# Kernel optimization log

Measured on AMD Instinct MI355X. Metric: run time of the kernel, lower is better.

## Reference

```python
import jax, jax.numpy as jnp
import numpy as np

N_NODES = 10000
N_GRAPHS = 64
NEG_SLOPE = 0.2
EPS = 1e-16


def gat_conv(x, src, dst, W, a_src, a_dst, bias, heads, out_ch, num_nodes):
    """PyG GATConv (shared lin, add_self_loops already applied to src/dst)."""
    xl = (x @ W).reshape(num_nodes, heads, out_ch)          # [N,H,C]
    alpha_s = jnp.einsum('nhc,hc->nh', xl, a_src)           # [N,H]
    alpha_d = jnp.einsum('nhc,hc->nh', xl, a_dst)           # [N,H]
    e = jax.nn.leaky_relu(alpha_s[src] + alpha_d[dst], NEG_SLOPE)  # [E,H]
    # segment softmax over incoming edges of each destination node
    emax = jax.ops.segment_max(e, dst, num_segments=num_nodes)
    emax = jnp.where(jnp.isfinite(emax), emax, 0.0)
    ee = jnp.exp(e - emax[dst])
    denom = jax.ops.segment_sum(ee, dst, num_segments=num_nodes)
    alpha = ee / (denom[dst] + EPS)                         # [E,H]
    msg = xl[src] * alpha[:, :, None]                       # [E,H,C]
    out = jax.ops.segment_sum(msg, dst, num_segments=num_nodes)  # [N,H,C]
    return out.reshape(num_nodes, heads * out_ch) + bias


def setup_inputs() -> dict:
    key = jax.random.key(0)
    ks = jax.random.split(key, 16)
    H, C, IN = 8, 128, 128
    x = jax.random.normal(ks[0], (N_NODES, IN), jnp.float32)
    edge_index = jax.random.randint(ks[1], (2, 320000), 0, N_NODES, jnp.int64)
    batch = jnp.sort(jax.random.randint(ks[2], (N_NODES,), 0, N_GRAPHS, jnp.int64))
    g = lambda k, shp, fan: jax.random.normal(k, shp, jnp.float32) * (1.0 / np.sqrt(fan))
    return {
        'x': x, 'edge_index': edge_index, 'batch': batch,
        'W1': g(ks[3], (IN, H * C), IN),
        'a_src1': g(ks[4], (H, C), C), 'a_dst1': g(ks[5], (H, C), C),
        'b1': jnp.zeros((H * C,), jnp.float32),
        'W2': g(ks[6], (H * C, C), H * C),
        'a_src2': g(ks[7], (1, C), C), 'a_dst2': g(ks[8], (1, C), C),
        'b2': jnp.zeros((C,), jnp.float32),
        'lin1_w': g(ks[9], (C, 128), C), 'lin1_b': jnp.zeros((128,), jnp.float32),
        'lin2_w': g(ks[10], (128, 1), 128), 'lin2_b': jnp.zeros((1,), jnp.float32),
    }


def reference(x, edge_index, batch, W1, a_src1, a_dst1, b1, W2, a_src2, a_dst2, b2,
              lin1_w, lin1_b, lin2_w, lin2_b):
    loops = jnp.arange(N_NODES, dtype=edge_index.dtype)
    src = jnp.concatenate([edge_index[0], loops])
    dst = jnp.concatenate([edge_index[1], loops])
    h = jax.nn.elu(gat_conv(x, src, dst, W1, a_src1, a_dst1, b1, 8, 128, N_NODES))
    h = jax.nn.elu(gat_conv(h, src, dst, W2, a_src2, a_dst2, b2, 1, 128, N_NODES))
    # global mean pool over graphs
    sums = jax.ops.segment_sum(h, batch, num_segments=N_GRAPHS)
    cnts = jax.ops.segment_sum(jnp.ones((N_NODES,), h.dtype), batch, num_segments=N_GRAPHS)
    pooled = sums / jnp.maximum(cnts, 1.0)[:, None]         # [G,128]
    z = jax.nn.relu(pooled @ lin1_w + lin1_b)
    return (z @ lin2_w + lin2_b).squeeze(1)                 # [G]
```

## Files before the change

### kernel.cpp

```cpp
#include <hip/hip_runtime.h>
#include <math.h>

#define N_NODES 10000
#define N_GRAPHS 64
#define E_RAW 320000
#define E_ALL (E_RAW + N_NODES)
#define NEG_SLOPE 0.2f
#define EPS 1e-16f
#define CAP 192

typedef unsigned short ushort_t;
typedef short short8 __attribute__((ext_vector_type(8)));
typedef float floatx4 __attribute__((ext_vector_type(4)));

static __device__ __forceinline__ float bfl(unsigned u) {
  union { unsigned u; float f; } v; v.u = u << 16; return v.f;
}
static __device__ __forceinline__ float bfh(unsigned u) {
  union { unsigned u; float f; } v; v.u = u & 0xFFFF0000u; return v.f;
}
static __device__ __forceinline__ ushort_t f2bf(float f) {
  union { float f; unsigned u; } v; v.f = f;
  unsigned r = v.u + 0x7FFFu + ((v.u >> 16) & 1u);
  return (ushort_t)(r >> 16);
}

static __device__ __forceinline__ void load16_lds(const ushort_t* gp, ushort_t* ldsbase, int lane) {
#if __has_builtin(__builtin_amdgcn_global_load_lds)
  __builtin_amdgcn_global_load_lds((const __attribute__((address_space(1))) void*)gp,
                                   (__attribute__((address_space(3))) void*)ldsbase, 16, 0, 0);
#else
  *(uint4*)(ldsbase + lane * 8) = *(const uint4*)gp;
#endif
}

static __device__ __forceinline__ void swz_one(const float* __restrict__ W,
                                               ushort_t* __restrict__ Wsw,
                                               int idx, int K, int N) {
  int NT = N >> 4;
  int lane = idx & 63, tile = idx >> 6;
  int nt = tile % NT, kt = tile / NT;
  int n = nt * 16 + (lane & 15);
  int kb = kt * 32 + (lane >> 4) * 8;
  ushort4 lo, hi;
  lo.x = f2bf(W[(size_t)(kb + 0) * N + n]); lo.y = f2bf(W[(size_t)(kb + 1) * N + n]);
  lo.z = f2bf(W[(size_t)(kb + 2) * N + n]); lo.w = f2bf(W[(size_t)(kb + 3) * N + n]);
  hi.x = f2bf(W[(size_t)(kb + 4) * N + n]); hi.y = f2bf(W[(size_t)(kb + 5) * N + n]);
  hi.z = f2bf(W[(size_t)(kb + 6) * N + n]); hi.w = f2bf(W[(size_t)(kb + 7) * N + n]);
  *(ushort4*)(Wsw + (size_t)idx * 8) = lo;
  *(ushort4*)(Wsw + (size_t)idx * 8 + 4) = hi;
}

__global__ __launch_bounds__(1024) void prep_k(const float* __restrict__ x,
                                               const int* __restrict__ batch,
                                               const float* __restrict__ W1,
                                               const float* __restrict__ W2,
                                               ushort_t* __restrict__ xb,
                                               ushort_t* __restrict__ W1sw,
                                               ushort_t* __restrict__ W2sw,
                                               float* __restrict__ zero0,
                                               int* __restrict__ poolcnt) {
  __shared__ int shm[N_GRAPHS];
  const int b = blockIdx.x, t = threadIdx.x;
  if (b < 49) {
    int i4 = b * 1024 + t;
    if (i4 < 49548) *(float4*)(zero0 + i4 * 4) = make_float4(0.f, 0.f, 0.f, 0.f);
  } else if (b == 49) {
    if (t < N_GRAPHS) shm[t] = 0;
    __syncthreads();
    for (int n = t; n < N_NODES; n += 1024) atomicAdd(&shm[batch[n]], 1);
    __syncthreads();
    if (t < N_GRAPHS) poolcnt[t] = shm[t];
  } else if (b < 363) {
    int i4 = (b - 50) * 1024 + t;
    if (i4 < 320000) {
      float4 v = *(const float4*)(x + (size_t)i4 * 4);
      ushort4 o;
      o.x = f2bf(v.x); o.y = f2bf(v.y); o.z = f2bf(v.z); o.w = f2bf(v.w);
      *(ushort4*)(xb + (size_t)i4 * 4) = o;
    }
  } else if (b < 379) {
    int idx = (b - 363) * 1024 + t;
    if (idx < 16384) swz_one(W1, W1sw, idx, 128, 1024);
  } else {
    int idx = (b - 379) * 1024 + t;
    if (idx < 16384) swz_one(W2, W2sw, idx, 1024, 128);
  }
}

__global__ __launch_bounds__(256) void g1f_k(const ushort_t* __restrict__ A,
                                             const ushort_t* __restrict__ Bsw,
                                             ushort_t* __restrict__ Cb,
                                             const float* __restrict__ aS,
                                             const float* __restrict__ aD,
                                             float* __restrict__ asO,
                                             float* __restrict__ adO,
                                             const int* __restrict__ ei,
                                             int* __restrict__ degc,
                                             int* __restrict__ csr) {
  __shared__ ushort_t Albuf[32 * 512];
  __shared__ float epi[4][16][68];
  const int bid = blockIdx.x, t = threadIdx.x;
  if (bid >= 632) {
    int e = (bid - 632) * 256 + t;
    if (e < E_ALL) {
      int s, d;
      if (e < E_RAW) { s = ei[e]; d = ei[E_RAW + e]; }
      else           { s = d = e - E_RAW; }
      int pos = atomicAdd(&degc[d], 1);
      if (pos < CAP) csr[d * CAP + pos] = s;
    }
    return;
  }
  const int M = N_NODES, K = 128, NT = 64;
  const int lane = t & 63, w = t >> 6;
  const int wm = w >> 1, wn = w & 1;
  const int m0 = (bid >> 3) * 128;
  const int n0 = (bid & 7) * 128;
  const int g = lane >> 4, l16 = lane & 15;

  #pragma unroll
  for (int i = 0; i < 8; i++) {
    int tile = w * 8 + i;
    int mtl = tile >> 2, kt = tile & 3;
    int r = m0 + mtl * 16 + l16; r = r < M ? r : M - 1;
    load16_lds(A + (size_t)r * K + kt * 32 + g * 8, &Albuf[tile * 512], lane);
  }
  __syncthreads();

  floatx4 acc[4][4] = {};
  #pragma unroll
  for (int kt = 0; kt < 4; kt++) {
    short8 a[4], b[4];
    #pragma unroll
    for (int mi = 0; mi < 4; mi++)
      a[mi] = *(const short8*)&Albuf[(((wm * 4 + mi) * 4 + kt) * 64 + lane) * 8];
    #pragma unroll
    for (int ni = 0; ni < 4; ni++) {
      int nt = (n0 >> 4) + wn * 4 + ni;
      b[ni] = *(const short8*)(Bsw + ((size_t)(kt * NT + nt) * 64 + lane) * 8);
    }
    #pragma unroll
    for (int mi = 0; mi < 4; mi++)
      #pragma unroll
      for (int ni = 0; ni < 4; ni++)
        acc[mi][ni] = __builtin_amdgcn_mfma_f32_16x16x32_bf16(a[mi], b[ni], acc[mi][ni], 0, 0, 0);
  }

  const int h = bid & 7;
  const int r = lane >> 2, c0 = (lane & 3) * 16;
  const int colh = wn * 64 + c0;
  float asc[16], adc[16];
  #pragma unroll
  for (int c = 0; c < 16; c++) { asc[c] = aS[h * 128 + colh + c]; adc[c] = aD[h * 128 + colh + c]; }
  #pragma unroll
  for (int mi = 0; mi < 4; mi++) {
    #pragma unroll
    for (int ni = 0; ni < 4; ni++)
      #pragma unroll
      for (int reg = 0; reg < 4; reg++)
        epi[w][g * 4 + reg][ni * 16 + l16] = acc[mi][ni][reg];
    float4 v0 = *(float4*)&epi[w][r][c0];
    float4 v1 = *(float4*)&epi[w][r][c0 + 4];
    float4 v2 = *(float4*)&epi[w][r][c0 + 8];
    float4 v3 = *(float4*)&epi[w][r][c0 + 12];
    float vr[16] = {v0.x,v0.y,v0.z,v0.w, v1.x,v1.y,v1.z,v1.w,
                    v2.x,v2.y,v2.z,v2.w, v3.x,v3.y,v3.z,v3.w};
    int grow = m0 + wm * 64 + mi * 16 + r;
    float sp = 0.f, dp = 0.f;
    ushort_t hv[16];
    #pragma unroll
    for (int c = 0; c < 16; c++) {
      sp = fmaf(vr[c], asc[c], sp);
      dp = fmaf(vr[c], adc[c], dp);
      hv[c] = f2bf(vr[c]);
    }
    sp += __shfl_xor(sp, 1); sp += __shfl_xor(sp, 2);
    dp += __shfl_xor(dp, 1); dp += __shfl_xor(dp, 2);
    if (grow < M) {
      uint4 u0, u1;
      u0.x = (unsigned)hv[0] | ((unsigned)hv[1] << 16);
      u0.y = (unsigned)hv[2] | ((unsigned)hv[3] << 16);
      u0.z = (unsigned)hv[4] | ((unsigned)hv[5] << 16);
      u0.w = (unsigned)hv[6] | ((unsigned)hv[7] << 16);
      u1.x = (unsigned)hv[8] | ((unsigned)hv[9] << 16);
      u1.y = (unsigned)hv[10] | ((unsigned)hv[11] << 16);
      u1.z = (unsigned)hv[12] | ((unsigned)hv[13] << 16);
      u1.w = (unsigned)hv[14] | ((unsigned)hv[15] << 16);
      ushort_t* cp = Cb + (size_t)grow * 1024 + (bid & 7) * 128 + wn * 64 + c0;
      *(uint4*)cp = u0;
      *(uint4*)(cp + 8) = u1;
      if ((lane & 3) == 0) {
        atomicAdd(&asO[grow * 8 + h], sp);
        atomicAdd(&adO[grow * 8 + h], dp);
      }
    }
  }
}

__global__ __launch_bounds__(256) void gemm2_k(const ushort_t* __restrict__ A,
                                               const ushort_t* __restrict__ Bsw,
                                               ushort_t* __restrict__ Cb,
                                               const float* __restrict__ aS,
                                               const float* __restrict__ aD,
                                               float* __restrict__ asO,
                                               float* __restrict__ adO) {
  const int M = N_NODES, K = 1024, NT = 8;
  __shared__ ushort_t Albuf[8 * 512];
  __shared__ float epi[4][16][68];
  const int t = threadIdx.x, lane = t & 63, w = t >> 6;
  const int wm = w >> 1, wn = w & 1;
  const int mb0 = blockIdx.x * 32;
  const int g = lane >> 4, l16 = lane & 15;

  floatx4 acc[4] = {};
  for (int ch = 0; ch < 8; ch++) {
    #pragma unroll
    for (int i = 0; i < 2; i++) {
      int tile = w * 2 + i;
      int mtl = tile >> 2, kt = tile & 3;
      int r = mb0 + mtl * 16 + l16; r = r < M ? r : M - 1;
      load16_lds(A + (size_t)r * K + (ch * 4 + kt) * 32 + g * 8, &Albuf[tile * 512], lane);
    }
    __syncthreads();
    #pragma unroll
    for (int ks = 0; ks < 4; ks++) {
      short8 a = *(const short8*)&Albuf[(((wm * 4 + ks)) * 64 + lane) * 8];
      #pragma unroll
      for (int ni = 0; ni < 4; ni++) {
        int nt = wn * 4 + ni, ktg = ch * 4 + ks;
        short8 b = *(const short8*)(Bsw + ((size_t)(ktg * NT + nt) * 64 + lane) * 8);
        acc[ni] = __builtin_amdgcn_mfma_f32_16x16x32_bf16(a, b, acc[ni], 0, 0, 0);
      }
    }
    __syncthreads();
  }

  const int r = lane >> 2, c0 = (lane & 3) * 16;
  const int colh = wn * 64 + c0;
  float asc[16], adc[16];
  #pragma unroll
  for (int c = 0; c < 16; c++) { asc[c] = aS[colh + c]; adc[c] = aD[colh + c]; }
  #pragma unroll
  for (int ni = 0; ni < 4; ni++)
    #pragma unroll
    for (int reg = 0; reg < 4; reg++)
      epi[w][g * 4 + reg][ni * 16 + l16] = acc[ni][reg];
  float4 v0 = *(float4*)&epi[w][r][c0];
  float4 v1 = *(float4*)&epi[w][r][c0 + 4];
  float4 v2 = *(float4*)&epi[w][r][c0 + 8];
  float4 v3 = *(float4*)&epi[w][r][c0 + 12];
  float vr[16] = {v0.x,v0.y,v0.z,v0.w, v1.x,v1.y,v1.z,v1.w,
                  v2.x,v2.y,v2.z,v2.w, v3.x,v3.y,v3.z,v3.w};
  int grow = mb0 + wm * 16 + r;
  float sp = 0.f, dp = 0.f;
  ushort_t hv[16];
  #pragma unroll
  for (int c = 0; c < 16; c++) {
    sp = fmaf(vr[c], asc[c], sp);
    dp = fmaf(vr[c], adc[c], dp);
    hv[c] = f2bf(vr[c]);
  }
  sp += __shfl_xor(sp, 1); sp += __shfl_xor(sp, 2);
  dp += __shfl_xor(dp, 1); dp += __shfl_xor(dp, 2);
  if (grow < M) {
    uint4 u0, u1;
    u0.x = (unsigned)hv[0] | ((unsigned)hv[1] << 16);
    u0.y = (unsigned)hv[2] | ((unsigned)hv[3] << 16);
    u0.z = (unsigned)hv[4] | ((unsigned)hv[5] << 16);
    u0.w = (unsigned)hv[6] | ((unsigned)hv[7] << 16);
    u1.x = (unsigned)hv[8] | ((unsigned)hv[9] << 16);
    u1.y = (unsigned)hv[10] | ((unsigned)hv[11] << 16);
    u1.z = (unsigned)hv[12] | ((unsigned)hv[13] << 16);
    u1.w = (unsigned)hv[14] | ((unsigned)hv[15] << 16);
    ushort_t* cp = Cb + (size_t)grow * 128 + colh;
    *(uint4*)cp = u0;
    *(uint4*)(cp + 8) = u1;
    if ((lane & 3) == 0) {
      atomicAdd(&asO[grow], sp);
      atomicAdd(&adO[grow], dp);
    }
  }
}

__global__ __launch_bounds__(64) void agg1_k(const ushort_t* __restrict__ xlb,
                                             const float* __restrict__ as1,
                                             const float* __restrict__ ad1,
                                             const float* __restrict__ b1,
                                             const int* __restrict__ degc,
                                             const int* __restrict__ csr,
                                             ushort_t* __restrict__ out) {
  const int bid = blockIdx.x, t = threadIdx.x;
  const int h = bid & 7, dst = bid >> 3;
  int deg = degc[dst]; deg = deg < CAP ? deg : CAP;
  const int beg = dst * CAP;
  const int degp = (deg + 7) & ~7;
  __shared__ uint2 pr[CAP];
  float adh = ad1[dst * 8 + h];
  if (deg <= 64) {
    bool act = t < deg;
    int s = act ? csr[beg + t] : 0;
    float lg = -1e30f;
    if (act) {
      float v = as1[s * 8 + h] + adh;
      lg = v > 0.f ? v : NEG_SLOPE * v;
    }
    float pm = lg;
    #pragma unroll
    for (int off = 32; off; off >>= 1) pm = fmaxf(pm, __shfl_xor(pm, off));
    float ex = act ? __expf(lg - pm) : 0.f;
    float ps = ex;
    #pragma unroll
    for (int off = 32; off; off >>= 1) ps += __shfl_xor(ps, off);
    float inv = 1.0f / (ps + EPS);
    if (t < degp) pr[t] = act ? make_uint2((unsigned)(s * 2048), __float_as_uint(ex * inv))
                              : make_uint2(0u, 0u);
    __syncthreads();
  } else {
    __shared__ int ssg[CAP];
    __shared__ float alg[CAP];
    for (int e = t; e < deg; e += 64) ssg[e] = csr[beg + e];
    __syncthreads();
    float pm = -1e30f;
    for (int e = t; e < deg; e += 64) {
      float v = as1[ssg[e] * 8 + h] + adh;
      v = v > 0.f ? v : NEG_SLOPE * v;
      alg[e] = v;
      pm = fmaxf(pm, v);
    }
    #pragma unroll
    for (int off = 32; off; off >>= 1) pm = fmaxf(pm, __shfl_xor(pm, off));
    __syncthreads();
    float ps = 0.f;
    for (int e = t; e < deg; e += 64) ps += __expf(alg[e] - pm);
    #pragma unroll
    for (int off = 32; off; off >>= 1) ps += __shfl_xor(ps, off);
    float inv = 1.0f / (ps + EPS);
    for (int e = t; e < deg; e += 64)
      pr[e] = make_uint2((unsigned)(ssg[e] * 2048), __float_as_uint(__expf(alg[e] - pm) * inv));
    for (int e = deg + t; e < degp; e += 64) pr[e] = make_uint2(0u, 0u);
    __syncthreads();
  }
  const int g = t >> 4, sub = t & 15;
  const char* xbase = (const char*)xlb + (h * 256 + 16 * sub);
  float acc[8] = {};
  for (int e0 = 0; e0 < degp; e0 += 8) {
    uint2 pA = pr[e0 + g];
    uint2 pB = pr[e0 + 4 + g];
    uint4 qA = *(const uint4*)(xbase + pA.x);
    uint4 qB = *(const uint4*)(xbase + pB.x);
    float aA = __uint_as_float(pA.y), aB = __uint_as_float(pB.y);
    acc[0] = fmaf(aA, bfl(qA.x), acc[0]); acc[1] = fmaf(aA, bfh(qA.x), acc[1]);
    acc[2] = fmaf(aA, bfl(qA.y), acc[2]); acc[3] = fmaf(aA, bfh(qA.y), acc[3]);
    acc[4] = fmaf(aA, bfl(qA.z), acc[4]); acc[5] = fmaf(aA, bfh(qA.z), acc[5]);
    acc[6] = fmaf(aA, bfl(qA.w), acc[6]); acc[7] = fmaf(aA, bfh(qA.w), acc[7]);
    acc[0] = fmaf(aB, bfl(qB.x), acc[0]); acc[1] = fmaf(aB, bfh(qB.x), acc[1]);
    acc[2] = fmaf(aB, bfl(qB.y), acc[2]); acc[3] = fmaf(aB, bfh(qB.y), acc[3]);
    acc[4] = fmaf(aB, bfl(qB.z), acc[4]); acc[5] = fmaf(aB, bfh(qB.z), acc[5]);
    acc[6] = fmaf(aB, bfl(qB.w), acc[6]); acc[7] = fmaf(aB, bfh(qB.w), acc[7]);
  }
  const bool hi32 = (t & 32) != 0;
  float s0, s1, s2, s3;
  {
    float m0 = hi32 ? acc[4] : acc[0], o0 = hi32 ? acc[0] : acc[4];
    float m1 = hi32 ? acc[5] : acc[1], o1 = hi32 ? acc[1] : acc[5];
    float m2 = hi32 ? acc[6] : acc[2], o2 = hi32 ? acc[2] : acc[6];
    float m3 = hi32 ? acc[7] : acc[3], o3 = hi32 ? acc[3] : acc[7];
    s0 = m0 + __shfl_xor(o0, 32);
    s1 = m1 + __shfl_xor(o1, 32);
    s2 = m2 + __shfl_xor(o2, 32);
    s3 = m3 + __shfl_xor(o3, 32);
  }
  const bool hi16 = (t & 16) != 0;
  float r0, r1;
  {
    float m0 = hi16 ? s2 : s0, o0 = hi16 ? s0 : s2;
    float m1 = hi16 ? s3 : s1, o1 = hi16 ? s1 : s3;
    r0 = m0 + __shfl_xor(o0, 16);
    r1 = m1 + __shfl_xor(o1, 16);
  }
  const int c = 8 * sub + 2 * g;
  const int o = h * 128 + c;
  float2 bb = *(const float2*)(b1 + o);
  float v0 = r0 + bb.x;
  float v1 = r1 + bb.y;
  v0 = v0 > 0.f ? v0 : (__expf(v0) - 1.0f);
  v1 = v1 > 0.f ? v1 : (__expf(v1) - 1.0f);
  unsigned up = (unsigned)f2bf(v0) | ((unsigned)f2bf(v1) << 16);
  *(unsigned*)(out + (size_t)dst * 1024 + o) = up;
}

__global__ __launch_bounds__(64) void agg2_k(const ushort_t* __restrict__ xlb2,
                                             const float* __restrict__ as2,
                                             const float* __restrict__ ad2,
                                             const float* __restrict__ b2,
                                             const int* __restrict__ degc,
                                             const int* __restrict__ csr,
                                             const int* __restrict__ batch,
                                             float* __restrict__ poolsum) {
  int dst = blockIdx.x, t = threadIdx.x;
  int deg = degc[dst]; deg = deg < CAP ? deg : CAP;
  int beg = dst * CAP;
  const int degp = (deg + 7) & ~7;
  float adv = ad2[dst];
  __shared__ uint2 pr[CAP];
  if (deg <= 64) {
    bool act = t < deg;
    int s = act ? csr[beg + t] : 0;
    float lg = -1e30f;
    if (act) {
      float v = as2[s] + adv;
      lg = v > 0.f ? v : NEG_SLOPE * v;
    }
    float pm = lg;
    #pragma unroll
    for (int off = 32; off; off >>= 1) pm = fmaxf(pm, __shfl_xor(pm, off));
    float ex = act ? __expf(lg - pm) : 0.f;
    float ps = ex;
    #pragma unroll
    for (int off = 32; off; off >>= 1) ps += __shfl_xor(ps, off);
    float inv = 1.0f / (ps + EPS);
    if (t < degp) pr[t] = act ? make_uint2((unsigned)(s * 256), __float_as_uint(ex * inv))
                              : make_uint2(0u, 0u);
    __syncthreads();
  } else {
    __shared__ int ssg[CAP];
    __shared__ float alg[CAP];
    for (int e = t; e < deg; e += 64) ssg[e] = csr[beg + e];
    __syncthreads();
    float pm = -1e30f;
    for (int e = t; e < deg; e += 64) {
      float v = as2[ssg[e]] + adv;
      v = v > 0.f ? v : NEG_SLOPE * v;
      alg[e] = v;
      pm = fmaxf(pm, v);
    }
    #pragma unroll
    for (int off = 32; off; off >>= 1) pm = fmaxf(pm, __shfl_xor(pm, off));
    __syncthreads();
    float ps = 0.f;
    for (int e = t; e < deg; e += 64) ps += __expf(alg[e] - pm);
    #pragma unroll
    for (int off = 32; off; off >>= 1) ps += __shfl_xor(ps, off);
    float inv = 1.0f / (ps + EPS);
    for (int e = t; e < deg; e += 64)
      pr[e] = make_uint2((unsigned)(ssg[e] * 256), __float_as_uint(__expf(alg[e] - pm) * inv));
    for (int e = deg + t; e < degp; e += 64) pr[e] = make_uint2(0u, 0u);
    __syncthreads();
  }
  const int g = t >> 4, sub = t & 15;
  const char* xbase = (const char*)xlb2 + 16 * sub;
  float acc[8] = {};
  for (int e0 = 0; e0 < degp; e0 += 8) {
    uint2 pA = pr[e0 + g];
    uint2 pB = pr[e0 + 4 + g];
    uint4 qA = *(const uint4*)(xbase + pA.x);
    uint4 qB = *(const uint4*)(xbase + pB.x);
    float aA = __uint_as_float(pA.y), aB = __uint_as_float(pB.y);
    acc[0] = fmaf(aA, bfl(qA.x), acc[0]); acc[1] = fmaf(aA, bfh(qA.x), acc[1]);
    acc[2] = fmaf(aA, bfl(qA.y), acc[2]); acc[3] = fmaf(aA, bfh(qA.y), acc[3]);
    acc[4] = fmaf(aA, bfl(qA.z), acc[4]); acc[5] = fmaf(aA, bfh(qA.z), acc[5]);
    acc[6] = fmaf(aA, bfl(qA.w), acc[6]); acc[7] = fmaf(aA, bfh(qA.w), acc[7]);
    acc[0] = fmaf(aB, bfl(qB.x), acc[0]); acc[1] = fmaf(aB, bfh(qB.x), acc[1]);
    acc[2] = fmaf(aB, bfl(qB.y), acc[2]); acc[3] = fmaf(aB, bfh(qB.y), acc[3]);
    acc[4] = fmaf(aB, bfl(qB.z), acc[4]); acc[5] = fmaf(aB, bfh(qB.z), acc[5]);
    acc[6] = fmaf(aB, bfl(qB.w), acc[6]); acc[7] = fmaf(aB, bfh(qB.w), acc[7]);
  }
  const bool hi32 = (t & 32) != 0;
  float s0, s1, s2, s3;
  {
    float m0 = hi32 ? acc[4] : acc[0], o0 = hi32 ? acc[0] : acc[4];
    float m1 = hi32 ? acc[5] : acc[1], o1 = hi32 ? acc[1] : acc[5];
    float m2 = hi32 ? acc[6] : acc[2], o2 = hi32 ? acc[2] : acc[6];
    float m3 = hi32 ? acc[7] : acc[3], o3 = hi32 ? acc[3] : acc[7];
    s0 = m0 + __shfl_xor(o0, 32);
    s1 = m1 + __shfl_xor(o1, 32);
    s2 = m2 + __shfl_xor(o2, 32);
    s3 = m3 + __shfl_xor(o3, 32);
  }
  const bool hi16 = (t & 16) != 0;
  float r0, r1;
  {
    float m0 = hi16 ? s2 : s0, o0 = hi16 ? s0 : s2;
    float m1 = hi16 ? s3 : s1, o1 = hi16 ? s1 : s3;
    r0 = m0 + __shfl_xor(o0, 16);
    r1 = m1 + __shfl_xor(o1, 16);
  }
  const int c0 = 8 * sub + 2 * g;
  float2 bb = *(const float2*)(b2 + c0);
  float v0 = r0 + bb.x;
  float v1 = r1 + bb.y;
  v0 = v0 > 0.f ? v0 : (__expf(v0) - 1.0f);
  v1 = v1 > 0.f ? v1 : (__expf(v1) - 1.0f);
  int gb = batch[dst];
  atomicAdd(&poolsum[gb * 128 + c0], v0);
  atomicAdd(&poolsum[gb * 128 + c0 + 1], v1);
}

__global__ __launch_bounds__(128) void final_k(const float* __restrict__ poolsum,
                                               const int* __restrict__ cnt,
                                               const float* __restrict__ l1w,
                                               const float* __restrict__ l1b,
                                               const float* __restrict__ l2w,
                                               const float* __restrict__ l2b,
                                               float* __restrict__ out) {
  int g = blockIdx.x, t = threadIdx.x;
  __shared__ float pooled[128];
  float c = fmaxf((float)cnt[g], 1.0f);
  pooled[t] = poolsum[g * 128 + t] / c;
  __syncthreads();
  float acc = l1b[t];
  for (int i = 0; i < 128; i++) acc = fmaf(pooled[i], l1w[i * 128 + t], acc);
  acc = fmaxf(acc, 0.0f);
  float p = acc * l2w[t];
  #pragma unroll
  for (int off = 32; off; off >>= 1) p += __shfl_down(p, off);
  __shared__ float r[2];
  if ((t & 63) == 0) r[t >> 6] = p;
  __syncthreads();
  if (t == 0) out[g] = r[0] + r[1] + l2b[0];
}

extern "C" void kernel_launch(void* const* d_in, const int* in_sizes, int n_in,
                              void* d_out, int out_size, void* d_ws, size_t ws_size,
                              hipStream_t stream) {
  const float* x    = (const float*)d_in[0];
  const int*   ei   = (const int*)d_in[1];
  const int*   batch= (const int*)d_in[2];
  const float* W1   = (const float*)d_in[3];
  const float* aS1  = (const float*)d_in[4];
  const float* aD1  = (const float*)d_in[5];
  const float* b1   = (const float*)d_in[6];
  const float* W2   = (const float*)d_in[7];
  const float* aS2  = (const float*)d_in[8];
  const float* aD2  = (const float*)d_in[9];
  const float* b2   = (const float*)d_in[10];
  const float* l1w  = (const float*)d_in[11];
  const float* l1b  = (const float*)d_in[12];
  const float* l2w  = (const float*)d_in[13];
  const float* l2b  = (const float*)d_in[14];
  float* out = (float*)d_out;

  ushort_t* xlb1   = (ushort_t*)d_ws;
  ushort_t* h1b    = xlb1 + 10240000;
  ushort_t* xlb2   = h1b + 10240000;
  ushort_t* xb     = xlb2 + 1280000;
  ushort_t* W1sw   = xb + 1280000;
  ushort_t* W2sw   = W1sw + 131072;
  float*    zero0  = (float*)(W2sw + 131072);
  float*    as1    = zero0;
  float*    ad1    = as1 + 80000;
  float*    as2    = ad1 + 80000;
  float*    ad2    = as2 + 10000;
  float*    poolsum= ad2 + 10000;
  int*      degc   = (int*)(poolsum + 8192);
  int*      poolcnt= degc + 10000;
  int*      csr    = poolcnt + 64;

  prep_k<<<395, 1024, 0, stream>>>(x, batch, W1, W2, xb, W1sw, W2sw, zero0, poolcnt);
  g1f_k<<<632 + 1290, 256, 0, stream>>>(xb, W1sw, xlb1, aS1, aD1, as1, ad1, ei, degc, csr);
  agg1_k<<<N_NODES * 8, 64, 0, stream>>>(xlb1, as1, ad1, b1, degc, csr, h1b);
  gemm2_k<<<313, 256, 0, stream>>>(h1b, W2sw, xlb2, aS2, aD2, as2, ad2);
  agg2_k<<<N_NODES, 64, 0, stream>>>(xlb2, as2, ad2, b2, degc, csr, batch, poolsum);
  final_k<<<N_GRAPHS, 128, 0, stream>>>(poolsum, poolcnt, l1w, l1b, l2w, l2b, out);
}
```

Before: 216.4 us.

## Pack two destination nodes per block and software-pipeline gather loads in aggregation

Both aggregation kernels now run two independent 64-lane waves per 128-thread block, each handling its own destination node with per-wave shared buffers. Because each wave only touches its own slice, the block-wide barriers are dropped. The gather loop is also software-pipelined: the next pair of edge records and feature rows is loaded before the FMAs on the current pair, to hide global-load latency. This halves the block count and removes barrier stalls, at the cost of more registers and relying on intra-wave ordering of shared memory without explicit barriers.

```diff
diff --git a/kernel.cpp b/kernel.cpp
--- a/kernel.cpp
+++ b/kernel.cpp
@@ -283,23 +283,31 @@
   }
 }
 
-__global__ __launch_bounds__(64) void agg1_k(const ushort_t* __restrict__ xlb,
-                                             const float* __restrict__ as1,
-                                             const float* __restrict__ ad1,
-                                             const float* __restrict__ b1,
-                                             const int* __restrict__ degc,
-                                             const int* __restrict__ csr,
-                                             ushort_t* __restrict__ out) {
+#define FMA8W(q, a) \
+  acc[0] = fmaf(a, bfl(q.x), acc[0]); acc[1] = fmaf(a, bfh(q.x), acc[1]); \
+  acc[2] = fmaf(a, bfl(q.y), acc[2]); acc[3] = fmaf(a, bfh(q.y), acc[3]); \
+  acc[4] = fmaf(a, bfl(q.z), acc[4]); acc[5] = fmaf(a, bfh(q.z), acc[5]); \
+  acc[6] = fmaf(a, bfl(q.w), acc[6]); acc[7] = fmaf(a, bfh(q.w), acc[7]);
+
+__global__ __launch_bounds__(128) void agg1_k(const ushort_t* __restrict__ xlb,
+                                              const float* __restrict__ as1,
+                                              const float* __restrict__ ad1,
+                                              const float* __restrict__ b1,
+                                              const int* __restrict__ degc,
+                                              const int* __restrict__ csr,
+                                              ushort_t* __restrict__ out) {
   const int bid = blockIdx.x, t = threadIdx.x;
-  const int h = bid & 7, dst = bid >> 3;
+  const int lane = t & 63, wv = t >> 6;
+  const int h = bid & 7, dst = (bid >> 3) * 2 + wv;
   int deg = degc[dst]; deg = deg < CAP ? deg : CAP;
   const int beg = dst * CAP;
   const int degp = (deg + 7) & ~7;
-  __shared__ uint2 pr[CAP];
+  __shared__ uint2 pr[2][CAP];
+  uint2* prw = pr[wv];
   float adh = ad1[dst * 8 + h];
   if (deg <= 64) {
-    bool act = t < deg;
-    int s = act ? csr[beg + t] : 0;
+    bool act = lane < deg;
+    int s = act ? csr[beg + lane] : 0;
     float lg = -1e30f;
     if (act) {
       float v = as1[s * 8 + h] + adh;
@@ -313,53 +321,54 @@
     #pragma unroll
     for (int off = 32; off; off >>= 1) ps += __shfl_xor(ps, off);
     float inv = 1.0f / (ps + EPS);
-    if (t < degp) pr[t] = act ? make_uint2((unsigned)(s * 2048), __float_as_uint(ex * inv))
-                              : make_uint2(0u, 0u);
-    __syncthreads();
+    if (lane < degp) prw[lane] = act ? make_uint2((unsigned)(s * 2048), __float_as_uint(ex * inv))
+                                     : make_uint2(0u, 0u);
   } else {
-    __shared__ int ssg[CAP];
-    __shared__ float alg[CAP];
-    for (int e = t; e < deg; e += 64) ssg[e] = csr[beg + e];
-    __syncthreads();
+    __shared__ int ssg[2][CAP];
+    __shared__ float alg[2][CAP];
+    int* ss = ssg[wv]; float* al = alg[wv];
+    for (int e = lane; e < deg; e += 64) ss[e] = csr[beg + e];
     float pm = -1e30f;
-    for (int e = t; e < deg; e += 64) {
-      float v = as1[ssg[e] * 8 + h] + adh;
+    for (int e = lane; e < deg; e += 64) {
+      float v = as1[ss[e] * 8 + h] + adh;
       v = v > 0.f ? v : NEG_SLOPE * v;
-      alg[e] = v;
+      al[e] = v;
       pm = fmaxf(pm, v);
     }
     #pragma unroll
     for (int off = 32; off; off >>= 1) pm = fmaxf(pm, __shfl_xor(pm, off));
-    __syncthreads();
     float ps = 0.f;
-    for (int e = t; e < deg; e += 64) ps += __expf(alg[e] - pm);
+    for (int e = lane; e < deg; e += 64) ps += __expf(al[e] - pm);
     #pragma unroll
     for (int off = 32; off; off >>= 1) ps += __shfl_xor(ps, off);
     float inv = 1.0f / (ps + EPS);
-    for (int e = t; e < deg; e += 64)
-      pr[e] = make_uint2((unsigned)(ssg[e] * 2048), __float_as_uint(__expf(alg[e] - pm) * inv));
-    for (int e = deg + t; e < degp; e += 64) pr[e] = make_uint2(0u, 0u);
-    __syncthreads();
-  }
-  const int g = t >> 4, sub = t & 15;
-  const char* xbase = (const char*)xlb + (h * 256 + 16 * sub);
+    for (int e = lane; e < deg; e += 64)
+      prw[e] = make_uint2((unsigned)(ss[e] * 2048), __float_as_uint(__expf(al[e] - pm) * inv));
+    for (int e = deg + lane; e < degp; e += 64) prw[e] = make_uint2(0u, 0u);
+  }
+  const int g = lane >> 4, sub = lane & 15;
+  const unsigned lanoff = (unsigned)(h * 256 + 16 * sub);
+  const char* xbase = (const char*)xlb;
+  const uint2* prg = prw + g;
   float acc[8] = {};
-  for (int e0 = 0; e0 < degp; e0 += 8) {
-    uint2 pA = pr[e0 + g];
-    uint2 pB = pr[e0 + 4 + g];
-    uint4 qA = *(const uint4*)(xbase + pA.x);
-    uint4 qB = *(const uint4*)(xbase + pB.x);
+  uint2 pA = prg[0], pB = prg[4];
+  uint4 qA = *(const uint4*)(xbase + (pA.x + lanoff));
+  uint4 qB = *(const uint4*)(xbase + (pB.x + lanoff));
+  for (int e0 = 8; e0 < degp; e0 += 8) {
+    uint2 pA2 = prg[e0], pB2 = prg[e0 + 4];
+    uint4 qA2 = *(const uint4*)(xbase + (pA2.x + lanoff));
+    uint4 qB2 = *(const uint4*)(xbase + (pB2.x + lanoff));
     float aA = __uint_as_float(pA.y), aB = __uint_as_float(pB.y);
-    acc[0] = fmaf(aA, bfl(qA.x), acc[0]); acc[1] = fmaf(aA, bfh(qA.x), acc[1]);
-    acc[2] = fmaf(aA, bfl(qA.y), acc[2]); acc[3] = fmaf(aA, bfh(qA.y), acc[3]);
-    acc[4] = fmaf(aA, bfl(qA.z), acc[4]); acc[5] = fmaf(aA, bfh(qA.z), acc[5]);
-    acc[6] = fmaf(aA, bfl(qA.w), acc[6]); acc[7] = fmaf(aA, bfh(qA.w), acc[7]);
-    acc[0] = fmaf(aB, bfl(qB.x), acc[0]); acc[1] = fmaf(aB, bfh(qB.x), acc[1]);
-    acc[2] = fmaf(aB, bfl(qB.y), acc[2]); acc[3] = fmaf(aB, bfh(qB.y), acc[3]);
-    acc[4] = fmaf(aB, bfl(qB.z), acc[4]); acc[5] = fmaf(aB, bfh(qB.z), acc[5]);
-    acc[6] = fmaf(aB, bfl(qB.w), acc[6]); acc[7] = fmaf(aB, bfh(qB.w), acc[7]);
-  }
-  const bool hi32 = (t & 32) != 0;
+    FMA8W(qA, aA);
+    FMA8W(qB, aB);
+    pA = pA2; pB = pB2; qA = qA2; qB = qB2;
+  }
+  {
+    float aA = __uint_as_float(pA.y), aB = __uint_as_float(pB.y);
+    FMA8W(qA, aA);
+    FMA8W(qB, aB);
+  }
+  const bool hi32 = (lane & 32) != 0;
   float s0, s1, s2, s3;
   {
     float m0 = hi32 ? acc[4] : acc[0], o0 = hi32 ? acc[0] : acc[4];
@@ -371,7 +380,7 @@
     s2 = m2 + __shfl_xor(o2, 32);
     s3 = m3 + __shfl_xor(o3, 32);
   }
-  const bool hi16 = (t & 16) != 0;
+  const bool hi16 = (lane & 16) != 0;
   float r0, r1;
   {
     float m0 = hi16 ? s2 : s0, o0 = hi16 ? s0 : s2;
@@ -390,23 +399,26 @@
   *(unsigned*)(out + (size_t)dst * 1024 + o) = up;
 }
 
-__global__ __launch_bounds__(64) void agg2_k(const ushort_t* __restrict__ xlb2,
-                                             const float* __restrict__ as2,
-                                             const float* __restrict__ ad2,
-                                             const float* __restrict__ b2,
-                                             const int* __restrict__ degc,
-                                             const int* __restrict__ csr,
-                                             const int* __restrict__ batch,
-                                             float* __restrict__ poolsum) {
-  int dst = blockIdx.x, t = threadIdx.x;
+__global__ __launch_bounds__(128) void agg2_k(const ushort_t* __restrict__ xlb2,
+                                              const float* __restrict__ as2,
+                                              const float* __restrict__ ad2,
+                                              const float* __restrict__ b2,
+                                              const int* __restrict__ degc,
+                                              const int* __restrict__ csr,
+                                              const int* __restrict__ batch,
+                                              float* __restrict__ poolsum) {
+  const int bid = blockIdx.x, t = threadIdx.x;
+  const int lane = t & 63, wv = t >> 6;
+  const int dst = bid * 2 + wv;
   int deg = degc[dst]; deg = deg < CAP ? deg : CAP;
   int beg = dst * CAP;
   const int degp = (deg + 7) & ~7;
   float adv = ad2[dst];
-  __shared__ uint2 pr[CAP];
+  __shared__ uint2 pr[2][CAP];
+  uint2* prw = pr[wv];
   if (deg <= 64) {
-    bool act = t < deg;
-    int s = act ? csr[beg + t] : 0;
+    bool act = lane < deg;
+    int s = act ? csr[beg + lane] : 0;
     float lg = -1e30f;
     if (act) {
       float v = as2[s] + adv;
@@ -420,53 +432,54 @@
     #pragma unroll
     for (int off = 32; off; off >>= 1) ps += __shfl_xor(ps, off);
     float inv = 1.0f / (ps + EPS);
-    if (t < degp) pr[t] = act ? make_uint2((unsigned)(s * 256), __float_as_uint(ex * inv))
-                              : make_uint2(0u, 0u);
-    __syncthreads();
+    if (lane < degp) prw[lane] = act ? make_uint2((unsigned)(s * 256), __float_as_uint(ex * inv))
+                                     : make_uint2(0u, 0u);
   } else {
-    __shared__ int ssg[CAP];
-    __shared__ float alg[CAP];
-    for (int e = t; e < deg; e += 64) ssg[e] = csr[beg + e];
-    __syncthreads();
+    __shared__ int ssg[2][CAP];
+    __shared__ float alg[2][CAP];
+    int* ss = ssg[wv]; float* al = alg[wv];
+    for (int e = lane; e < deg; e += 64) ss[e] = csr[beg + e];
     float pm = -1e30f;
-    for (int e = t; e < deg; e += 64) {
-      float v = as2[ssg[e]] + adv;
+    for (int e = lane; e < deg; e += 64) {
+      float v = as2[ss[e]] + adv;
       v = v > 0.f ? v : NEG_SLOPE * v;
-      alg[e] = v;
+      al[e] = v;
       pm = fmaxf(pm, v);
     }
     #pragma unroll
     for (int off = 32; off; off >>= 1) pm = fmaxf(pm, __shfl_xor(pm, off));
-    __syncthreads();
     float ps = 0.f;
-    for (int e = t; e < deg; e += 64) ps += __expf(alg[e] - pm);
+    for (int e = lane; e < deg; e += 64) ps += __expf(al[e] - pm);
     #pragma unroll
     for (int off = 32; off; off >>= 1) ps += __shfl_xor(ps, off);
     float inv = 1.0f / (ps + EPS);
-    for (int e = t; e < deg; e += 64)
-      pr[e] = make_uint2((unsigned)(ssg[e] * 256), __float_as_uint(__expf(alg[e] - pm) * inv));
-    for (int e = deg + t; e < degp; e += 64) pr[e] = make_uint2(0u, 0u);
-    __syncthreads();
-  }
-  const int g = t >> 4, sub = t & 15;
-  const char* xbase = (const char*)xlb2 + 16 * sub;
+    for (int e = lane; e < deg; e += 64)
+      prw[e] = make_uint2((unsigned)(ss[e] * 256), __float_as_uint(__expf(al[e] - pm) * inv));
+    for (int e = deg + lane; e < degp; e += 64) prw[e] = make_uint2(0u, 0u);
+  }
+  const int g = lane >> 4, sub = lane & 15;
+  const unsigned lanoff = (unsigned)(16 * sub);
+  const char* xbase = (const char*)xlb2;
+  const uint2* prg = prw + g;
   float acc[8] = {};
-  for (int e0 = 0; e0 < degp; e0 += 8) {
-    uint2 pA = pr[e0 + g];
-    uint2 pB = pr[e0 + 4 + g];
-    uint4 qA = *(const uint4*)(xbase + pA.x);
-    uint4 qB = *(const uint4*)(xbase + pB.x);
+  uint2 pA = prg[0], pB = prg[4];
+  uint4 qA = *(const uint4*)(xbase + (pA.x + lanoff));
+  uint4 qB = *(const uint4*)(xbase + (pB.x + lanoff));
+  for (int e0 = 8; e0 < degp; e0 += 8) {
+    uint2 pA2 = prg[e0], pB2 = prg[e0 + 4];
+    uint4 qA2 = *(const uint4*)(xbase + (pA2.x + lanoff));
+    uint4 qB2 = *(const uint4*)(xbase + (pB2.x + lanoff));
     float aA = __uint_as_float(pA.y), aB = __uint_as_float(pB.y);
-    acc[0] = fmaf(aA, bfl(qA.x), acc[0]); acc[1] = fmaf(aA, bfh(qA.x), acc[1]);
-    acc[2] = fmaf(aA, bfl(qA.y), acc[2]); acc[3] = fmaf(aA, bfh(qA.y), acc[3]);
-    acc[4] = fmaf(aA, bfl(qA.z), acc[4]); acc[5] = fmaf(aA, bfh(qA.z), acc[5]);
-    acc[6] = fmaf(aA, bfl(qA.w), acc[6]); acc[7] = fmaf(aA, bfh(qA.w), acc[7]);
-    acc[0] = fmaf(aB, bfl(qB.x), acc[0]); acc[1] = fmaf(aB, bfh(qB.x), acc[1]);
-    acc[2] = fmaf(aB, bfl(qB.y), acc[2]); acc[3] = fmaf(aB, bfh(qB.y), acc[3]);
-    acc[4] = fmaf(aB, bfl(qB.z), acc[4]); acc[5] = fmaf(aB, bfh(qB.z), acc[5]);
-    acc[6] = fmaf(aB, bfl(qB.w), acc[6]); acc[7] = fmaf(aB, bfh(qB.w), acc[7]);
-  }
-  const bool hi32 = (t & 32) != 0;
+    FMA8W(qA, aA);
+    FMA8W(qB, aB);
+    pA = pA2; pB = pB2; qA = qA2; qB = qB2;
+  }
+  {
+    float aA = __uint_as_float(pA.y), aB = __uint_as_float(pB.y);
+    FMA8W(qA, aA);
+    FMA8W(qB, aB);
+  }
+  const bool hi32 = (lane & 32) != 0;
   float s0, s1, s2, s3;
   {
     float m0 = hi32 ? acc[4] : acc[0], o0 = hi32 ? acc[0] : acc[4];
@@ -478,7 +491,7 @@
     s2 = m2 + __shfl_xor(o2, 32);
     s3 = m3 + __shfl_xor(o3, 32);
   }
-  const bool hi16 = (t & 16) != 0;
+  const bool hi16 = (lane & 16) != 0;
   float r0, r1;
   {
     float m0 = hi16 ? s2 : s0, o0 = hi16 ? s0 : s2;
@@ -559,8 +572,8 @@
 
   prep_k<<<395, 1024, 0, stream>>>(x, batch, W1, W2, xb, W1sw, W2sw, zero0, poolcnt);
   g1f_k<<<632 + 1290, 256, 0, stream>>>(xb, W1sw, xlb1, aS1, aD1, as1, ad1, ei, degc, csr);
-  agg1_k<<<N_NODES * 8, 64, 0, stream>>>(xlb1, as1, ad1, b1, degc, csr, h1b);
+  agg1_k<<<(N_NODES / 2) * 8, 128, 0, stream>>>(xlb1, as1, ad1, b1, degc, csr, h1b);
   gemm2_k<<<313, 256, 0, stream>>>(h1b, W2sw, xlb2, aS2, aD2, as2, ad2);
-  agg2_k<<<N_NODES, 64, 0, stream>>>(xlb2, as2, ad2, b2, degc, csr, batch, poolsum);
+  agg2_k<<<N_NODES / 2, 128, 0, stream>>>(xlb2, as2, ad2, b2, degc, csr, batch, poolsum);
   final_k<<<N_GRAPHS, 128, 0, stream>>>(poolsum, poolcnt, l1w, l1b, l2w, l2b, out);
 }
```

New measurement: 219.9 us. About the same (+1.6%).
